# Kernel optimization log

Hardware: AMD Instinct MI355X
Metric: run time of the kernel (lower is better)

## Reference

```python
import jax, jax.numpy as jnp
import numpy as np
import math

ROW, COL, DIM, ORDER, K, E = 10000, 4096, 16, 3, 5, 1000000
V = ORDER + 1  # var_size = order + 1
BIG = 100000.0


def setup_inputs() -> dict:
    key = jax.random.key(0)
    ks = jax.random.split(key, 10)
    u = lambda k, s: 2.0 * jax.random.uniform(k, s, dtype=jnp.float32) - 1.0
    z_rows = u(ks[0], (V, ROW, DIM))
    z_cols = u(ks[1], (COL, DIM))
    gamma_rows = u(ks[2], (ROW,))
    gamma_cols = u(ks[3], (COL,))
    L = jnp.tril(u(ks[4], (COL, DIM, DIM)))  # 'full' metric_param: lower-triangular per column
    b = jnp.asarray(np.linspace(-1.0, 1.0, K - 1), dtype=jnp.float32).at[(K - 1) // 2].set(0.0)
    sigma = jnp.ones((1,), jnp.float32)
    col_times = jax.random.uniform(ks[5], (COL,), dtype=jnp.float32)
    mat_rows = jax.random.randint(ks[6], (E,), 0, ROW, dtype=jnp.int32)
    mat_cols = jax.random.randint(ks[7], (E,), 0, COL, dtype=jnp.int32)
    y = jax.random.randint(ks[8], (E,), 1, K + 1, dtype=jnp.int32)  # event values 1..class_num
    col_idx_list = jax.random.randint(ks[9], (COL,), 0, COL, dtype=jnp.int32)
    return dict(z_rows=z_rows, z_cols=z_cols, gamma_rows=gamma_rows, gamma_cols=gamma_cols,
                L=L, b=b, sigma=sigma, col_times=col_times,
                mat_rows=mat_rows, mat_cols=mat_cols, y=y, col_idx_list=col_idx_list)


def reference(z_rows, z_cols, gamma_rows, gamma_cols, L, b, sigma, col_times,
              mat_rows, mat_cols, y, col_idx_list):
    # polynomial time features: tpow[o, c] = t_c**o / o!
    facts = jnp.asarray([math.factorial(o) for o in range(V)], jnp.float32)
    orders = jnp.arange(V, dtype=jnp.float32)
    tpow = col_times[None, :] ** orders[:, None] / facts[:, None]      # (V, COL)
    # per-event row positions: z_e = sum_o z_rows[o, r_e] * t_{c_e}^o / o!
    zr = z_rows[:, mat_rows, :]                                        # (V, E, D)
    tp = tpow[:, mat_cols]                                             # (V, E)
    z = jnp.einsum('ved,ve->ed', zr, tp)                               # (E, D)
    # Mahalanobis distance: || delta @ L[col_idx_list[c]] ||_2
    delta = z - z_cols[mat_cols]                                       # (E, D)
    Lg = L[col_idx_list[mat_cols]]                                     # (E, D, D)
    T = jnp.einsum('ed,edk->ek', delta, Lg)                            # (E, D)
    dist = jnp.linalg.norm(T, axis=1)                                  # (E,)
    f = -dist + gamma_rows[mat_rows] + gamma_cols[mat_cols]
    # ordinal likelihood via probit thresholds theta = [-BIG, b..., BIG]
    theta = jnp.concatenate([jnp.asarray([-BIG], jnp.float32), b, jnp.asarray([BIG], jnp.float32)])
    cdf = jax.scipy.stats.norm.cdf
    s = sigma[0]
    ll = jnp.log(cdf((theta[y] - f) / s) - cdf((theta[y - 1] - f) / s))
    return -jnp.sum(ll)
```

## Files before the change

kernel.cpp:

```cpp
#include <hip/hip_runtime.h>
#include <math.h>

#define ROWN 10000
#define COLN 4096
#define DIM 16
#define EN 1000000
#define BIGF 100000.0f

#define RECQ 48
#define RECF (RECQ * 4)

#define NBT 40
#define RPT 250
#define NBH 64
#define CHH 15625
#define NBS 250
#define CHS 4000

__constant__ int QK[40] = {0,0,0,0, 1,1,1,1, 2,2,2,2, 3,3,3,3,
                           4,4,4, 5,5,5, 6,6,6, 7,7,7,
                           8,8, 9,9, 10,10, 11,11, 12, 13, 14, 15};
__constant__ int QQ[40] = {0,1,2,3, 0,1,2,3, 0,1,2,3, 0,1,2,3,
                           1,2,3, 1,2,3, 1,2,3, 1,2,3,
                           2,3, 2,3, 2,3, 2,3, 3, 3, 3, 3};

__host__ __device__ __forceinline__ constexpr int offk(int k) {
    return (k < 4) ? k * 4
         : (k < 8) ? 16 + (k - 4) * 3
         : (k < 12) ? 28 + (k - 8) * 2
         : 36 + (k - 12);
}

__global__ __launch_bounds__(256) void init3(
    const float* __restrict__ z_rows, const float* __restrict__ z_cols,
    const float* __restrict__ gamma_cols, const float* __restrict__ L,
    const float* __restrict__ col_times, const int* __restrict__ col_idx_list,
    float* __restrict__ rec, float* __restrict__ zt,
    const int* __restrict__ mc, int* __restrict__ gcnt)
{
    const int tid = threadIdx.x;
    if (blockIdx.x < NBT) {
        const int r0 = blockIdx.x * RPT;
        const size_t SL = (size_t)ROWN * DIM;
        float4* dst = (float4*)zt;
        #pragma unroll
        for (int v = 0; v < 4; ++v) {
            const float4* src = (const float4*)(z_rows + (size_t)v * SL
                                                + (size_t)r0 * DIM);
            for (int idx = tid; idx < RPT * 4; idx += 256) {
                const int r = idx >> 2, q = idx & 3;
                dst[(size_t)(r0 + r) * 16 + v * 4 + q] = src[idx];
            }
        }
    } else if (blockIdx.x < NBT + NBH) {
        __shared__ int h[COLN];
        const int b = blockIdx.x - NBT;
        for (int i = tid; i < COLN; i += 256) h[i] = 0;
        __syncthreads();
        const int lo = b * CHH, hi = min(lo + CHH, EN);
        for (int e = lo + tid; e < hi; e += 256)
            atomicAdd(&h[mc[e]], 1);
        __syncthreads();
        for (int i = tid; i < COLN; i += 256) {
            int v = h[i];
            if (v) atomicAdd(&gcnt[i], v);
        }
    } else {
        __shared__ float Lsh[DIM][DIM + 1];
        const int c = blockIdx.x - (NBT + NBH);
        const int cidx = col_idx_list[c];
        Lsh[tid >> 4][tid & 15] = L[(size_t)cidx * 256 + tid];
        __syncthreads();

        float4* r = (float4*)(rec + (size_t)c * RECF);
        if (tid < 40) {
            const int k = QK[tid];
            const int d = 4 * QQ[tid];
            r[1 + tid] = make_float4(Lsh[d][k], Lsh[d+1][k], Lsh[d+2][k], Lsh[d+3][k]);
        } else if (tid < 44) {
            const int j = tid - 40;
            const float* zp = z_cols + (size_t)c * DIM + 4 * j;
            r[41 + j] = make_float4(zp[0], zp[1], zp[2], zp[3]);
        } else if (tid == 44) {
            const float t = col_times[c];
            r[0]  = make_float4(1.0f, t, 0.5f * t * t, t * t * t * (1.0f / 6.0f));
            r[45] = make_float4(gamma_cols[c], 0.0f, 0.0f, 0.0f);
        }
    }
}

__global__ __launch_bounds__(512) void scatter3(
    const int* __restrict__ mr, const int* __restrict__ mc,
    const int* __restrict__ yy, const int* __restrict__ gcnt,
    int* __restrict__ gcur, int* __restrict__ gbase,
    int* __restrict__ packed)
{
    __shared__ int bases[COLN];
    __shared__ int lh[COLN];
    __shared__ int sums[512];
    const int tid = threadIdx.x;

    int s = 0;
    #pragma unroll
    for (int i = 0; i < 8; ++i) {
        int c = tid * 8 + i;
        int v = gcnt[c];
        bases[c] = v;
        s += v;
    }
    sums[tid] = s;
    __syncthreads();
    for (int off = 1; off < 512; off <<= 1) {
        int v = (tid >= off) ? sums[tid - off] : 0;
        __syncthreads();
        sums[tid] += v;
        __syncthreads();
    }
    int run = (tid == 0) ? 0 : sums[tid - 1];
    #pragma unroll
    for (int i = 0; i < 8; ++i) {
        int c = tid * 8 + i;
        int v = bases[c];
        bases[c] = run;
        run += v;
    }
    if (blockIdx.x == 0) {
        #pragma unroll
        for (int i = 0; i < 8; ++i) { int c = tid * 8 + i; gbase[c] = bases[c]; }
    }

    for (int i = tid; i < COLN; i += 512) lh[i] = 0;
    __syncthreads();
    const int b = blockIdx.x;
    const int lo = b * CHS, hi = min(lo + CHS, EN);
    for (int e = lo + tid; e < hi; e += 512)
        atomicAdd(&lh[mc[e]], 1);
    __syncthreads();

    for (int i = tid; i < COLN; i += 512) {
        int cntl = lh[i];
        if (cntl) lh[i] = bases[i] + atomicAdd(&gcur[i], cntl);
    }
    __syncthreads();

    for (int e = lo + tid; e < hi; e += 512) {
        int c = mc[e];
        int pos = atomicAdd(&lh[c], 1);
        packed[pos] = mr[e] | (yy[e] << 14);
    }
}

__device__ __forceinline__ float log_cdf_diff_f(float hi, float lo) {
    const float r = 0.70710678118654752440f;
    if (hi + lo < 0.0f) { float t = hi; hi = -lo; lo = -t; }
    float d = erfcf(lo * r) - erfcf(hi * r);
    return logf(0.5f * fmaxf(d, 1e-37f));
}

__global__ __launch_bounds__(128) void edge4(
    const float* __restrict__ zt, const float* __restrict__ gamma_rows,
    const float4* __restrict__ rec4, const float* __restrict__ b,
    const float* __restrict__ sigma, const int* __restrict__ packed,
    const int* __restrict__ gbase, const int* __restrict__ gcnt,
    double* __restrict__ bsum)
{
    __shared__ float4 R[RECQ];
    __shared__ float th[6];
    __shared__ double wsum[2];
    const int c = blockIdx.x;
    const int tid = threadIdx.x;
    if (tid < RECQ) R[tid] = rec4[(size_t)c * RECQ + tid];
    if (tid == 0) { th[0] = -BIGF; th[5] = BIGF; }
    if (tid < 4)  th[1 + tid] = b[tid];
    __syncthreads();

    const float inv_s = 1.0f / sigma[0];
    const int base = gbase[c];
    const int cnt  = gcnt[c];
    const float4 t0 = R[0];
    const float tp1 = t0.y, tp2 = t0.z, tp3 = t0.w;
    const float4 zc0 = R[41], zc1 = R[42], zc2 = R[43], zc3 = R[44];
    const float gcol = R[45].x;

    double acc = 0.0;
    for (int i = tid; i < cnt; i += 128) {
        const int p   = packed[base + i];
        const int row = p & 0x3FFF;
        const int yv  = (p >> 14) & 7;
        const float4* zp = (const float4*)(zt + (size_t)row * 64);

        float4 a[16];
        #pragma unroll
        for (int j = 0; j < 16; ++j) a[j] = zp[j];
        const float ga = gamma_rows[row];

        float d_[DIM];
        #pragma unroll
        for (int q = 0; q < 4; ++q) {
            const float4 zc = (q == 0) ? zc0 : (q == 1) ? zc1 : (q == 2) ? zc2 : zc3;
            d_[4*q+0] = fmaf(a[12+q].x, tp3, fmaf(a[8+q].x, tp2, fmaf(a[4+q].x, tp1, a[q].x))) - zc.x;
            d_[4*q+1] = fmaf(a[12+q].y, tp3, fmaf(a[8+q].y, tp2, fmaf(a[4+q].y, tp1, a[q].y))) - zc.y;
            d_[4*q+2] = fmaf(a[12+q].z, tp3, fmaf(a[8+q].z, tp2, fmaf(a[4+q].z, tp1, a[q].z))) - zc.z;
            d_[4*q+3] = fmaf(a[12+q].w, tp3, fmaf(a[8+q].w, tp2, fmaf(a[4+q].w, tp1, a[q].w))) - zc.w;
        }

        float nsq = 0.0f;
        #pragma unroll
        for (int k = 0; k < DIM; ++k) {
            const int q0 = k >> 2;
            float t = 0.0f;
            #pragma unroll
            for (int q = q0; q < 4; ++q) {
                const float4 lv = R[1 + offk(k) + (q - q0)];
                t = fmaf(lv.x, d_[4*q+0],
                    fmaf(lv.y, d_[4*q+1],
                    fmaf(lv.z, d_[4*q+2],
                    fmaf(lv.w, d_[4*q+3], t))));
            }
            nsq = fmaf(t, t, nsq);
        }

        const float f = ga + gcol - sqrtf(nsq);
        acc += (double)log_cdf_diff_f((th[yv] - f) * inv_s,
                                      (th[yv - 1] - f) * inv_s);
    }

    #pragma unroll
    for (int off = 32; off > 0; off >>= 1) acc += __shfl_down(acc, off, 64);
    const int lane = tid & 63;
    const int wid  = tid >> 6;
    if (lane == 0) wsum[wid] = acc;
    __syncthreads();
    if (tid == 0) bsum[c] = wsum[0] + wsum[1];
}

__global__ __launch_bounds__(512) void finalize2(const double* __restrict__ bsum,
                                                 float* __restrict__ out)
{
    __shared__ double s[512];
    const int tid = threadIdx.x;
    double a = 0.0;
    #pragma unroll
    for (int i = 0; i < 8; ++i) a += bsum[tid * 8 + i];
    s[tid] = a;
    __syncthreads();
    for (int off = 256; off > 0; off >>= 1) {
        if (tid < off) s[tid] += s[tid + off];
        __syncthreads();
    }
    if (tid == 0) out[0] = -(float)s[0];
}

extern "C" void kernel_launch(void* const* d_in, const int* in_sizes, int n_in,
                              void* d_out, int out_size, void* d_ws, size_t ws_size,
                              hipStream_t stream) {
    const float* z_rows       = (const float*)d_in[0];
    const float* z_cols       = (const float*)d_in[1];
    const float* gamma_rows   = (const float*)d_in[2];
    const float* gamma_cols   = (const float*)d_in[3];
    const float* L            = (const float*)d_in[4];
    const float* b            = (const float*)d_in[5];
    const float* sigma        = (const float*)d_in[6];
    const float* col_times    = (const float*)d_in[7];
    const int*   mat_rows     = (const int*)d_in[8];
    const int*   mat_cols     = (const int*)d_in[9];
    const int*   y            = (const int*)d_in[10];
    const int*   col_idx_list = (const int*)d_in[11];

    char* ws = (char*)d_ws;
    float*  rec   = (float*)ws;
    float*  zt    = (float*)(ws + 3145728);
    int*    gcnt  = (int*)(ws + 5705728);
    int*    gbase = (int*)(ws + 5722112);
    int*    gcur  = (int*)(ws + 5738496);
    double* bsum  = (double*)(ws + 5754880);
    int*    pk    = (int*)(ws + 5787648);

    hipMemsetAsync(gcnt, 0, 3 * 16384, stream);
    init3<<<NBT + NBH + COLN, 256, 0, stream>>>(
        z_rows, z_cols, gamma_cols, L, col_times, col_idx_list, rec, zt,
        mat_cols, gcnt);
    scatter3<<<NBS, 512, 0, stream>>>(mat_rows, mat_cols, y, gcnt, gcur, gbase, pk);
    edge4<<<COLN, 128, 0, stream>>>(zt, gamma_rows, (const float4*)rec,
                                    b, sigma, pk, gbase, gcnt, bsum);
    finalize2<<<1, 512, 0, stream>>>(bsum, (float*)d_out);
}
```

Baseline: 171.4 us.

## Process four columns per edge block, prefetch packed entries, fuse final reduction

Each edge block now handles four consecutive columns' edges as one contiguous range, with the column-within-group encoded in the packed word. This balances the uneven per-column edge counts and removes the tail waste of small 128-thread blocks. The next packed entry is prefetched during the current iteration. The separate finalize kernel is replaced by a last-block-done atomic counter reduction, which saves a launch but adds threadfences and a per-thread shared-memory record indexed by column, and that indexing may cause bank conflicts.

```diff
diff --git a/kernel.cpp b/kernel.cpp
--- a/kernel.cpp
+++ b/kernel.cpp
@@ -16,6 +16,11 @@
 #define CHH 15625
 #define NBS 250
 #define CHS 4000
+
+#define CPB 4
+#define EBLK (COLN / CPB)
+
+struct Ctrl { int done; int pad; };
 
 __constant__ int QK[40] = {0,0,0,0, 1,1,1,1, 2,2,2,2, 3,3,3,3,
                            4,4,4, 5,5,5, 6,6,6, 7,7,7,
@@ -89,7 +94,7 @@
     }
 }
 
-__global__ __launch_bounds__(512) void scatter3(
+__global__ __launch_bounds__(512) void scatter4(
     const int* __restrict__ mr, const int* __restrict__ mc,
     const int* __restrict__ yy, const int* __restrict__ gcnt,
     int* __restrict__ gcur, int* __restrict__ gbase,
@@ -127,6 +132,7 @@
     if (blockIdx.x == 0) {
         #pragma unroll
         for (int i = 0; i < 8; ++i) { int c = tid * 8 + i; gbase[c] = bases[c]; }
+        if (tid == 511) gbase[COLN] = run;
     }
 
     for (int i = tid; i < COLN; i += 512) lh[i] = 0;
@@ -146,7 +152,7 @@
     for (int e = lo + tid; e < hi; e += 512) {
         int c = mc[e];
         int pos = atomicAdd(&lh[c], 1);
-        packed[pos] = mr[e] | (yy[e] << 14);
+        packed[pos] = mr[e] | (yy[e] << 14) | ((c & 3) << 17);
     }
 }
 
@@ -157,47 +163,54 @@
     return logf(0.5f * fmaxf(d, 1e-37f));
 }
 
-__global__ __launch_bounds__(128) void edge4(
+__global__ __launch_bounds__(256, 4) void edge5(
     const float* __restrict__ zt, const float* __restrict__ gamma_rows,
     const float4* __restrict__ rec4, const float* __restrict__ b,
     const float* __restrict__ sigma, const int* __restrict__ packed,
-    const int* __restrict__ gbase, const int* __restrict__ gcnt,
-    double* __restrict__ bsum)
+    const int* __restrict__ gbase, Ctrl* __restrict__ ctrl,
+    double* __restrict__ bsum, float* __restrict__ out)
 {
-    __shared__ float4 R[RECQ];
+    __shared__ float4 R[CPB * RECQ];
     __shared__ float th[6];
-    __shared__ double wsum[2];
-    const int c = blockIdx.x;
+    __shared__ double wsum[4];
+    __shared__ int lastf;
     const int tid = threadIdx.x;
-    if (tid < RECQ) R[tid] = rec4[(size_t)c * RECQ + tid];
+    const int c0 = blockIdx.x * CPB;
+    if (tid < CPB * RECQ) R[tid] = rec4[(size_t)c0 * RECQ + tid];
     if (tid == 0) { th[0] = -BIGF; th[5] = BIGF; }
     if (tid < 4)  th[1 + tid] = b[tid];
     __syncthreads();
 
     const float inv_s = 1.0f / sigma[0];
-    const int base = gbase[c];
-    const int cnt  = gcnt[c];
-    const float4 t0 = R[0];
-    const float tp1 = t0.y, tp2 = t0.z, tp3 = t0.w;
-    const float4 zc0 = R[41], zc1 = R[42], zc2 = R[43], zc3 = R[44];
-    const float gcol = R[45].x;
+    const int base = gbase[c0];
+    const int end  = gbase[c0 + CPB];
 
     double acc = 0.0;
-    for (int i = tid; i < cnt; i += 128) {
-        const int p   = packed[base + i];
+    int i = base + tid;
+    int p = 0;
+    if (i < end) p = packed[i];
+    for (; i < end; i += 256) {
         const int row = p & 0x3FFF;
         const int yv  = (p >> 14) & 7;
-        const float4* zp = (const float4*)(zt + (size_t)row * 64);
+        const int cl  = (p >> 17) & 3;
+        const float ga = gamma_rows[row];
+        const float4* __restrict__ zp = (const float4*)(zt + (size_t)row * 64);
 
         float4 a[16];
         #pragma unroll
         for (int j = 0; j < 16; ++j) a[j] = zp[j];
-        const float ga = gamma_rows[row];
+
+        int pn = 0;
+        if (i + 256 < end) pn = packed[i + 256];
+
+        const float4* __restrict__ Rc = &R[cl * RECQ];
+        const float4 t0 = Rc[0];
+        const float tp1 = t0.y, tp2 = t0.z, tp3 = t0.w;
 
         float d_[DIM];
         #pragma unroll
         for (int q = 0; q < 4; ++q) {
-            const float4 zc = (q == 0) ? zc0 : (q == 1) ? zc1 : (q == 2) ? zc2 : zc3;
+            const float4 zc = Rc[41 + q];
             d_[4*q+0] = fmaf(a[12+q].x, tp3, fmaf(a[8+q].x, tp2, fmaf(a[4+q].x, tp1, a[q].x))) - zc.x;
             d_[4*q+1] = fmaf(a[12+q].y, tp3, fmaf(a[8+q].y, tp2, fmaf(a[4+q].y, tp1, a[q].y))) - zc.y;
             d_[4*q+2] = fmaf(a[12+q].z, tp3, fmaf(a[8+q].z, tp2, fmaf(a[4+q].z, tp1, a[q].z))) - zc.z;
@@ -211,7 +224,7 @@
             float t = 0.0f;
             #pragma unroll
             for (int q = q0; q < 4; ++q) {
-                const float4 lv = R[1 + offk(k) + (q - q0)];
+                const float4 lv = Rc[1 + offk(k) + (q - q0)];
                 t = fmaf(lv.x, d_[4*q+0],
                     fmaf(lv.y, d_[4*q+1],
                     fmaf(lv.z, d_[4*q+2],
@@ -220,9 +233,10 @@
             nsq = fmaf(t, t, nsq);
         }
 
-        const float f = ga + gcol - sqrtf(nsq);
+        const float f = ga + Rc[45].x - sqrtf(nsq);
         acc += (double)log_cdf_diff_f((th[yv] - f) * inv_s,
                                       (th[yv - 1] - f) * inv_s);
+        p = pn;
     }
 
     #pragma unroll
@@ -231,24 +245,24 @@
     const int wid  = tid >> 6;
     if (lane == 0) wsum[wid] = acc;
     __syncthreads();
-    if (tid == 0) bsum[c] = wsum[0] + wsum[1];
-}
-
-__global__ __launch_bounds__(512) void finalize2(const double* __restrict__ bsum,
-                                                 float* __restrict__ out)
-{
-    __shared__ double s[512];
-    const int tid = threadIdx.x;
-    double a = 0.0;
-    #pragma unroll
-    for (int i = 0; i < 8; ++i) a += bsum[tid * 8 + i];
-    s[tid] = a;
-    __syncthreads();
-    for (int off = 256; off > 0; off >>= 1) {
-        if (tid < off) s[tid] += s[tid + off];
-        __syncthreads();
-    }
-    if (tid == 0) out[0] = -(float)s[0];
+    if (tid == 0) {
+        bsum[blockIdx.x] = wsum[0] + wsum[1] + wsum[2] + wsum[3];
+        __threadfence();
+        const int old = atomicAdd(&ctrl->done, 1);
+        lastf = (old == EBLK - 1);
+    }
+    __syncthreads();
+    if (lastf) {
+        __threadfence();
+        double a2 = 0.0;
+        #pragma unroll
+        for (int j = 0; j < EBLK / 256; ++j) a2 += bsum[tid + j * 256];
+        #pragma unroll
+        for (int off = 32; off > 0; off >>= 1) a2 += __shfl_down(a2, off, 64);
+        if (lane == 0) wsum[wid] = a2;
+        __syncthreads();
+        if (tid == 0) out[0] = -(float)(wsum[0] + wsum[1] + wsum[2] + wsum[3]);
+    }
 }
 
 extern "C" void kernel_launch(void* const* d_in, const int* in_sizes, int n_in,
@@ -271,17 +285,18 @@
     float*  rec   = (float*)ws;
     float*  zt    = (float*)(ws + 3145728);
     int*    gcnt  = (int*)(ws + 5705728);
-    int*    gbase = (int*)(ws + 5722112);
-    int*    gcur  = (int*)(ws + 5738496);
-    double* bsum  = (double*)(ws + 5754880);
-    int*    pk    = (int*)(ws + 5787648);
-
-    hipMemsetAsync(gcnt, 0, 3 * 16384, stream);
+    int*    gcur  = (int*)(ws + 5722112);
+    Ctrl*   ctrl  = (Ctrl*)(ws + 5738496);
+    int*    gbase = (int*)(ws + 5738624);
+    double* bsum  = (double*)(ws + 5755072);
+    int*    pk    = (int*)(ws + 5763264);
+
+    hipMemsetAsync(gcnt, 0, 2 * 16384 + 128, stream);
     init3<<<NBT + NBH + COLN, 256, 0, stream>>>(
         z_rows, z_cols, gamma_cols, L, col_times, col_idx_list, rec, zt,
         mat_cols, gcnt);
-    scatter3<<<NBS, 512, 0, stream>>>(mat_rows, mat_cols, y, gcnt, gcur, gbase, pk);
-    edge4<<<COLN, 128, 0, stream>>>(zt, gamma_rows, (const float4*)rec,
-                                    b, sigma, pk, gbase, gcnt, bsum);
-    finalize2<<<1, 512, 0, stream>>>(bsum, (float*)d_out);
-}
+    scatter4<<<NBS, 512, 0, stream>>>(mat_rows, mat_cols, y, gcnt, gcur, gbase, pk);
+    edge5<<<EBLK, 256, 0, stream>>>(zt, gamma_rows, (const float4*)rec,
+                                    b, sigma, pk, gbase, ctrl, bsum,
+                                    (float*)d_out);
+}
```

New measurement: 178.6 us. +4.2%, slower.

## Restructure stages: separate histogram, merge scatter with setup, fuse final reduction

Applied to the files above, without the earlier changes.

The column histogram now runs as its own kernel with 256 blocks instead of 64. The zt transpose and per-column record setup move into the scatter kernel, so they share one launch and overlap with the scatter blocks. The edge kernel handles two edges per thread per iteration and prefetches the next packed indices to hide gather latency. The finalize kernel is replaced by a last-block-done atomic reduction inside the edge kernel. This saves launches and adds latency hiding, at the cost of higher register pressure and a bigger mixed-block mid kernel with 512-thread blocks.

```diff
diff --git a/kernel.cpp b/kernel.cpp
--- a/kernel.cpp
+++ b/kernel.cpp
@@ -10,12 +10,14 @@
 #define RECQ 48
 #define RECF (RECQ * 4)
 
+#define NBH 256
+#define CHH 3907
+#define NBS 250
+#define CHS 4000
 #define NBT 40
 #define RPT 250
-#define NBH 64
-#define CHH 15625
-#define NBS 250
-#define CHS 4000
+
+struct Ctrl { int done; int pad; };
 
 __constant__ int QK[40] = {0,0,0,0, 1,1,1,1, 2,2,2,2, 3,3,3,3,
                            4,4,4, 5,5,5, 6,6,6, 7,7,7,
@@ -31,45 +33,104 @@
          : 36 + (k - 12);
 }
 
-__global__ __launch_bounds__(256) void init3(
+__global__ __launch_bounds__(256) void hist_k(
+    const int* __restrict__ mc, int* __restrict__ gcnt)
+{
+    __shared__ int h[COLN];
+    const int tid = threadIdx.x;
+    for (int i = tid; i < COLN; i += 256) h[i] = 0;
+    __syncthreads();
+    const int lo = blockIdx.x * CHH, hi = min(lo + CHH, EN);
+    for (int e = lo + tid; e < hi; e += 256)
+        atomicAdd(&h[mc[e]], 1);
+    __syncthreads();
+    for (int i = tid; i < COLN; i += 256) {
+        int v = h[i];
+        if (v) atomicAdd(&gcnt[i], v);
+    }
+}
+
+__global__ __launch_bounds__(512) void mid_k(
+    const int* __restrict__ mr, const int* __restrict__ mc,
+    const int* __restrict__ yy, const int* __restrict__ gcnt,
+    int* __restrict__ gcur, int* __restrict__ gbase,
+    int* __restrict__ packed,
     const float* __restrict__ z_rows, const float* __restrict__ z_cols,
     const float* __restrict__ gamma_cols, const float* __restrict__ L,
     const float* __restrict__ col_times, const int* __restrict__ col_idx_list,
-    float* __restrict__ rec, float* __restrict__ zt,
-    const int* __restrict__ mc, int* __restrict__ gcnt)
+    float* __restrict__ rec, float* __restrict__ zt)
 {
     const int tid = threadIdx.x;
-    if (blockIdx.x < NBT) {
-        const int r0 = blockIdx.x * RPT;
+    if (blockIdx.x < NBS) {
+        __shared__ int bases[COLN];
+        __shared__ int lh[COLN];
+        __shared__ int sums[512];
+
+        int s = 0;
+        #pragma unroll
+        for (int i = 0; i < 8; ++i) {
+            int c = tid * 8 + i;
+            int v = gcnt[c];
+            bases[c] = v;
+            s += v;
+        }
+        sums[tid] = s;
+        __syncthreads();
+        for (int off = 1; off < 512; off <<= 1) {
+            int v = (tid >= off) ? sums[tid - off] : 0;
+            __syncthreads();
+            sums[tid] += v;
+            __syncthreads();
+        }
+        int run = (tid == 0) ? 0 : sums[tid - 1];
+        #pragma unroll
+        for (int i = 0; i < 8; ++i) {
+            int c = tid * 8 + i;
+            int v = bases[c];
+            bases[c] = run;
+            run += v;
+        }
+        if (blockIdx.x == 0) {
+            #pragma unroll
+            for (int i = 0; i < 8; ++i) { int c = tid * 8 + i; gbase[c] = bases[c]; }
+        }
+
+        for (int i = tid; i < COLN; i += 512) lh[i] = 0;
+        __syncthreads();
+        const int lo = blockIdx.x * CHS, hi = min(lo + CHS, EN);
+        for (int e = lo + tid; e < hi; e += 512)
+            atomicAdd(&lh[mc[e]], 1);
+        __syncthreads();
+
+        for (int i = tid; i < COLN; i += 512) {
+            int cntl = lh[i];
+            if (cntl) lh[i] = bases[i] + atomicAdd(&gcur[i], cntl);
+        }
+        __syncthreads();
+
+        for (int e = lo + tid; e < hi; e += 512) {
+            int c = mc[e];
+            int pos = atomicAdd(&lh[c], 1);
+            packed[pos] = mr[e] | (yy[e] << 14);
+        }
+    } else if (blockIdx.x < NBS + NBT) {
+        const int r0 = (blockIdx.x - NBS) * RPT;
         const size_t SL = (size_t)ROWN * DIM;
         float4* dst = (float4*)zt;
         #pragma unroll
         for (int v = 0; v < 4; ++v) {
             const float4* src = (const float4*)(z_rows + (size_t)v * SL
                                                 + (size_t)r0 * DIM);
-            for (int idx = tid; idx < RPT * 4; idx += 256) {
+            for (int idx = tid; idx < RPT * 4; idx += 512) {
                 const int r = idx >> 2, q = idx & 3;
                 dst[(size_t)(r0 + r) * 16 + v * 4 + q] = src[idx];
             }
         }
-    } else if (blockIdx.x < NBT + NBH) {
-        __shared__ int h[COLN];
-        const int b = blockIdx.x - NBT;
-        for (int i = tid; i < COLN; i += 256) h[i] = 0;
-        __syncthreads();
-        const int lo = b * CHH, hi = min(lo + CHH, EN);
-        for (int e = lo + tid; e < hi; e += 256)
-            atomicAdd(&h[mc[e]], 1);
-        __syncthreads();
-        for (int i = tid; i < COLN; i += 256) {
-            int v = h[i];
-            if (v) atomicAdd(&gcnt[i], v);
-        }
     } else {
         __shared__ float Lsh[DIM][DIM + 1];
-        const int c = blockIdx.x - (NBT + NBH);
+        const int c = blockIdx.x - (NBS + NBT);
         const int cidx = col_idx_list[c];
-        Lsh[tid >> 4][tid & 15] = L[(size_t)cidx * 256 + tid];
+        if (tid < 256) Lsh[tid >> 4][tid & 15] = L[(size_t)cidx * 256 + tid];
         __syncthreads();
 
         float4* r = (float4*)(rec + (size_t)c * RECF);
@@ -89,67 +150,6 @@
     }
 }
 
-__global__ __launch_bounds__(512) void scatter3(
-    const int* __restrict__ mr, const int* __restrict__ mc,
-    const int* __restrict__ yy, const int* __restrict__ gcnt,
-    int* __restrict__ gcur, int* __restrict__ gbase,
-    int* __restrict__ packed)
-{
-    __shared__ int bases[COLN];
-    __shared__ int lh[COLN];
-    __shared__ int sums[512];
-    const int tid = threadIdx.x;
-
-    int s = 0;
-    #pragma unroll
-    for (int i = 0; i < 8; ++i) {
-        int c = tid * 8 + i;
-        int v = gcnt[c];
-        bases[c] = v;
-        s += v;
-    }
-    sums[tid] = s;
-    __syncthreads();
-    for (int off = 1; off < 512; off <<= 1) {
-        int v = (tid >= off) ? sums[tid - off] : 0;
-        __syncthreads();
-        sums[tid] += v;
-        __syncthreads();
-    }
-    int run = (tid == 0) ? 0 : sums[tid - 1];
-    #pragma unroll
-    for (int i = 0; i < 8; ++i) {
-        int c = tid * 8 + i;
-        int v = bases[c];
-        bases[c] = run;
-        run += v;
-    }
-    if (blockIdx.x == 0) {
-        #pragma unroll
-        for (int i = 0; i < 8; ++i) { int c = tid * 8 + i; gbase[c] = bases[c]; }
-    }
-
-    for (int i = tid; i < COLN; i += 512) lh[i] = 0;
-    __syncthreads();
-    const int b = blockIdx.x;
-    const int lo = b * CHS, hi = min(lo + CHS, EN);
-    for (int e = lo + tid; e < hi; e += 512)
-        atomicAdd(&lh[mc[e]], 1);
-    __syncthreads();
-
-    for (int i = tid; i < COLN; i += 512) {
-        int cntl = lh[i];
-        if (cntl) lh[i] = bases[i] + atomicAdd(&gcur[i], cntl);
-    }
-    __syncthreads();
-
-    for (int e = lo + tid; e < hi; e += 512) {
-        int c = mc[e];
-        int pos = atomicAdd(&lh[c], 1);
-        packed[pos] = mr[e] | (yy[e] << 14);
-    }
-}
-
 __device__ __forceinline__ float log_cdf_diff_f(float hi, float lo) {
     const float r = 0.70710678118654752440f;
     if (hi + lo < 0.0f) { float t = hi; hi = -lo; lo = -t; }
@@ -157,16 +157,53 @@
     return logf(0.5f * fmaxf(d, 1e-37f));
 }
 
-__global__ __launch_bounds__(128) void edge4(
+__device__ __forceinline__ double edge_ll(
+    const float4 a[16], const float4* __restrict__ R,
+    float tp1, float tp2, float tp3,
+    float4 zc0, float4 zc1, float4 zc2, float4 zc3,
+    float ga, float gcol, int yv, const float* __restrict__ th, float inv_s)
+{
+    float d_[DIM];
+    #pragma unroll
+    for (int q = 0; q < 4; ++q) {
+        const float4 zc = (q == 0) ? zc0 : (q == 1) ? zc1 : (q == 2) ? zc2 : zc3;
+        d_[4*q+0] = fmaf(a[12+q].x, tp3, fmaf(a[8+q].x, tp2, fmaf(a[4+q].x, tp1, a[q].x))) - zc.x;
+        d_[4*q+1] = fmaf(a[12+q].y, tp3, fmaf(a[8+q].y, tp2, fmaf(a[4+q].y, tp1, a[q].y))) - zc.y;
+        d_[4*q+2] = fmaf(a[12+q].z, tp3, fmaf(a[8+q].z, tp2, fmaf(a[4+q].z, tp1, a[q].z))) - zc.z;
+        d_[4*q+3] = fmaf(a[12+q].w, tp3, fmaf(a[8+q].w, tp2, fmaf(a[4+q].w, tp1, a[q].w))) - zc.w;
+    }
+    float nsq = 0.0f;
+    #pragma unroll
+    for (int k = 0; k < DIM; ++k) {
+        const int q0 = k >> 2;
+        float t = 0.0f;
+        #pragma unroll
+        for (int q = q0; q < 4; ++q) {
+            const float4 lv = R[1 + offk(k) + (q - q0)];
+            t = fmaf(lv.x, d_[4*q+0],
+                fmaf(lv.y, d_[4*q+1],
+                fmaf(lv.z, d_[4*q+2],
+                fmaf(lv.w, d_[4*q+3], t))));
+        }
+        nsq = fmaf(t, t, nsq);
+    }
+    const float f = ga + gcol - sqrtf(nsq);
+    return (double)log_cdf_diff_f((th[yv] - f) * inv_s,
+                                  (th[yv - 1] - f) * inv_s);
+}
+
+__global__ __launch_bounds__(128, 2) void edge6(
     const float* __restrict__ zt, const float* __restrict__ gamma_rows,
     const float4* __restrict__ rec4, const float* __restrict__ b,
     const float* __restrict__ sigma, const int* __restrict__ packed,
     const int* __restrict__ gbase, const int* __restrict__ gcnt,
-    double* __restrict__ bsum)
+    Ctrl* __restrict__ ctrl, double* __restrict__ bsum,
+    float* __restrict__ out)
 {
     __shared__ float4 R[RECQ];
     __shared__ float th[6];
     __shared__ double wsum[2];
+    __shared__ int lastf;
     const int c = blockIdx.x;
     const int tid = threadIdx.x;
     if (tid < RECQ) R[tid] = rec4[(size_t)c * RECQ + tid];
@@ -176,53 +213,49 @@
 
     const float inv_s = 1.0f / sigma[0];
     const int base = gbase[c];
-    const int cnt  = gcnt[c];
+    const int end  = base + gcnt[c];
     const float4 t0 = R[0];
     const float tp1 = t0.y, tp2 = t0.z, tp3 = t0.w;
     const float4 zc0 = R[41], zc1 = R[42], zc2 = R[43], zc3 = R[44];
     const float gcol = R[45].x;
 
     double acc = 0.0;
-    for (int i = tid; i < cnt; i += 128) {
-        const int p   = packed[base + i];
-        const int row = p & 0x3FFF;
-        const int yv  = (p >> 14) & 7;
-        const float4* zp = (const float4*)(zt + (size_t)row * 64);
-
-        float4 a[16];
-        #pragma unroll
-        for (int j = 0; j < 16; ++j) a[j] = zp[j];
-        const float ga = gamma_rows[row];
-
-        float d_[DIM];
-        #pragma unroll
-        for (int q = 0; q < 4; ++q) {
-            const float4 zc = (q == 0) ? zc0 : (q == 1) ? zc1 : (q == 2) ? zc2 : zc3;
-            d_[4*q+0] = fmaf(a[12+q].x, tp3, fmaf(a[8+q].x, tp2, fmaf(a[4+q].x, tp1, a[q].x))) - zc.x;
-            d_[4*q+1] = fmaf(a[12+q].y, tp3, fmaf(a[8+q].y, tp2, fmaf(a[4+q].y, tp1, a[q].y))) - zc.y;
-            d_[4*q+2] = fmaf(a[12+q].z, tp3, fmaf(a[8+q].z, tp2, fmaf(a[4+q].z, tp1, a[q].z))) - zc.z;
-            d_[4*q+3] = fmaf(a[12+q].w, tp3, fmaf(a[8+q].w, tp2, fmaf(a[4+q].w, tp1, a[q].w))) - zc.w;
-        }
-
-        float nsq = 0.0f;
-        #pragma unroll
-        for (int k = 0; k < DIM; ++k) {
-            const int q0 = k >> 2;
-            float t = 0.0f;
-            #pragma unroll
-            for (int q = q0; q < 4; ++q) {
-                const float4 lv = R[1 + offk(k) + (q - q0)];
-                t = fmaf(lv.x, d_[4*q+0],
-                    fmaf(lv.y, d_[4*q+1],
-                    fmaf(lv.z, d_[4*q+2],
-                    fmaf(lv.w, d_[4*q+3], t))));
-            }
-            nsq = fmaf(t, t, nsq);
-        }
-
-        const float f = ga + gcol - sqrtf(nsq);
-        acc += (double)log_cdf_diff_f((th[yv] - f) * inv_s,
-                                      (th[yv - 1] - f) * inv_s);
+    int i1 = base + tid;
+    int i2 = i1 + 128;
+    bool v1 = i1 < end;
+    bool v2 = i2 < end;
+    int p1 = 0, p2 = 0;
+    if (v1) p1 = packed[i1];
+    if (v2) p2 = packed[i2];
+    while (v1) {
+        const int row1 = p1 & 0x3FFF;
+        const int yv1  = (p1 >> 14) & 7;
+        const int row2 = v2 ? (p2 & 0x3FFF) : row1;
+        const int yv2  = (p2 >> 14) & 7;
+        const float ga1 = gamma_rows[row1];
+        const float ga2 = gamma_rows[row2];
+        const float4* __restrict__ zp1 = (const float4*)(zt + (size_t)row1 * 64);
+        const float4* __restrict__ zp2 = (const float4*)(zt + (size_t)row2 * 64);
+
+        float4 a1[16], a2[16];
+        #pragma unroll
+        for (int j = 0; j < 16; ++j) a1[j] = zp1[j];
+        #pragma unroll
+        for (int j = 0; j < 16; ++j) a2[j] = zp2[j];
+
+        const int i1n = i1 + 256, i2n = i2 + 256;
+        const bool v1n = i1n < end, v2n = i2n < end;
+        int p1n = 0, p2n = 0;
+        if (v1n) p1n = packed[i1n];
+        if (v2n) p2n = packed[i2n];
+
+        acc += edge_ll(a1, R, tp1, tp2, tp3, zc0, zc1, zc2, zc3,
+                       ga1, gcol, yv1, th, inv_s);
+        if (v2)
+            acc += edge_ll(a2, R, tp1, tp2, tp3, zc0, zc1, zc2, zc3,
+                           ga2, gcol, yv2, th, inv_s);
+
+        i1 = i1n; i2 = i2n; v1 = v1n; v2 = v2n; p1 = p1n; p2 = p2n;
     }
 
     #pragma unroll
@@ -231,24 +264,24 @@
     const int wid  = tid >> 6;
     if (lane == 0) wsum[wid] = acc;
     __syncthreads();
-    if (tid == 0) bsum[c] = wsum[0] + wsum[1];
-}
-
-__global__ __launch_bounds__(512) void finalize2(const double* __restrict__ bsum,
-                                                 float* __restrict__ out)
-{
-    __shared__ double s[512];
-    const int tid = threadIdx.x;
-    double a = 0.0;
-    #pragma unroll
-    for (int i = 0; i < 8; ++i) a += bsum[tid * 8 + i];
-    s[tid] = a;
-    __syncthreads();
-    for (int off = 256; off > 0; off >>= 1) {
-        if (tid < off) s[tid] += s[tid + off];
-        __syncthreads();
-    }
-    if (tid == 0) out[0] = -(float)s[0];
+    if (tid == 0) {
+        bsum[c] = wsum[0] + wsum[1];
+        __threadfence();
+        const int old = atomicAdd(&ctrl->done, 1);
+        lastf = (old == COLN - 1);
+    }
+    __syncthreads();
+    if (lastf) {
+        __threadfence();
+        double a2s = 0.0;
+        #pragma unroll
+        for (int j = 0; j < COLN / 128; ++j) a2s += bsum[tid + j * 128];
+        #pragma unroll
+        for (int off = 32; off > 0; off >>= 1) a2s += __shfl_down(a2s, off, 64);
+        if (lane == 0) wsum[wid] = a2s;
+        __syncthreads();
+        if (tid == 0) out[0] = -(float)(wsum[0] + wsum[1]);
+    }
 }
 
 extern "C" void kernel_launch(void* const* d_in, const int* in_sizes, int n_in,
@@ -271,17 +304,18 @@
     float*  rec   = (float*)ws;
     float*  zt    = (float*)(ws + 3145728);
     int*    gcnt  = (int*)(ws + 5705728);
-    int*    gbase = (int*)(ws + 5722112);
-    int*    gcur  = (int*)(ws + 5738496);
-    double* bsum  = (double*)(ws + 5754880);
-    int*    pk    = (int*)(ws + 5787648);
-
-    hipMemsetAsync(gcnt, 0, 3 * 16384, stream);
-    init3<<<NBT + NBH + COLN, 256, 0, stream>>>(
-        z_rows, z_cols, gamma_cols, L, col_times, col_idx_list, rec, zt,
-        mat_cols, gcnt);
-    scatter3<<<NBS, 512, 0, stream>>>(mat_rows, mat_cols, y, gcnt, gcur, gbase, pk);
-    edge4<<<COLN, 128, 0, stream>>>(zt, gamma_rows, (const float4*)rec,
-                                    b, sigma, pk, gbase, gcnt, bsum);
-    finalize2<<<1, 512, 0, stream>>>(bsum, (float*)d_out);
-}
+    int*    gcur  = (int*)(ws + 5722112);
+    Ctrl*   ctrl  = (Ctrl*)(ws + 5738496);
+    int*    gbase = (int*)(ws + 5738624);
+    double* bsum  = (double*)(ws + 5755008);
+    int*    pk    = (int*)(ws + 5787776);
+
+    hipMemsetAsync(gcnt, 0, 2 * 16384 + 128, stream);
+    hist_k<<<NBH, 256, 0, stream>>>(mat_cols, gcnt);
+    mid_k<<<NBS + NBT + COLN, 512, 0, stream>>>(
+        mat_rows, mat_cols, y, gcnt, gcur, gbase, pk,
+        z_rows, z_cols, gamma_cols, L, col_times, col_idx_list, rec, zt);
+    edge6<<<COLN, 128, 0, stream>>>(zt, gamma_rows, (const float4*)rec,
+                                    b, sigma, pk, gbase, gcnt, ctrl, bsum,
+                                    (float*)d_out);
+}
```

New measurement: 352.6 us. 2.06x slower.
